# Kernel tuning notes

Measured on AMD Instinct MI355X. Metric: run time of the kernel, lower is better.

The kernel has to match this reference:

```python
import jax, jax.numpy as jnp
import numpy as np

N_HEADS = 8
D_HEAD = 64  # n_embd=512 / n_heads=8


def setup_inputs() -> dict:
    key = jax.random.key(0)
    ks = jax.random.split(key, 5)
    B, T, C = 2, 4096, 512
    x = jax.random.normal(ks[0], (B, T, C), dtype=jnp.float32)
    s = 1.0 / np.sqrt(C)
    Wq = jax.random.normal(ks[1], (C, C), dtype=jnp.float32) * s
    Wk = jax.random.normal(ks[2], (C, C), dtype=jnp.float32) * s
    Wv = jax.random.normal(ks[3], (C, C), dtype=jnp.float32) * s
    Wout = jax.random.normal(ks[4], (C, C), dtype=jnp.float32) * s
    return {"x": x, "Wq": Wq, "Wk": Wk, "Wv": Wv, "Wout": Wout}


def reference(x, Wq, Wk, Wv, Wout):
    # x: [B,T,C]; nn.Linear(y) = y @ W.T, here weights stored as [C,C] used directly
    B, T, C = x.shape
    H, D = N_HEADS, D_HEAD
    q = (x @ Wq.T).reshape(B, T, H, D).transpose(0, 2, 1, 3)  # [B,H,T,D]
    k = (x @ Wk.T).reshape(B, T, H, D).transpose(0, 2, 1, 3)
    v = (x @ Wv.T).reshape(B, T, H, D).transpose(0, 2, 1, 3)
    att = jnp.einsum('bhqd,bhkd->bhqk', q, k) / jnp.sqrt(jnp.float32(D))  # [B,H,T,T]
    causal = jnp.tril(jnp.ones((T, T), dtype=bool))
    att = jnp.where(causal, att, -jnp.inf)
    att = jax.nn.softmax(att, axis=-1)
    # dropout is identity in eval mode (p=0)
    y = jnp.einsum('bhqk,bhkd->bhqd', att, v)  # [B,H,T,D]
    y = y.transpose(0, 2, 1, 3).reshape(B, T, C)
    return y @ Wout.T
```

## Files before the change

kernel.cpp:

```cpp
#include <hip/hip_runtime.h>
#include <hip/hip_bf16.h>
#include <math.h>
#include <stdint.h>

using bf16 = __hip_bfloat16;
typedef __attribute__((ext_vector_type(8))) short short8;
typedef __attribute__((ext_vector_type(4))) short short4v;
typedef __attribute__((ext_vector_type(4))) float float4v;

#define MFMA16(a, b, c) __builtin_amdgcn_mfma_f32_16x16x32_bf16(a, b, c, 0, 0, 0)

__device__ __forceinline__ short bfbits(float f) {
  bf16 h = (bf16)f;
  return *(short*)&h;
}

__device__ __forceinline__ short8 ld_cvt8(const float* p) {
  union { float4v v[2]; float f[8]; } u;
  u.v[0] = *(const float4v*)p;
  u.v[1] = *(const float4v*)(p + 4);
  short8 r;
#pragma unroll
  for (int j = 0; j < 8; j++) r[j] = bfbits(u.f[j]);
  return r;
}

__device__ __forceinline__ void gload16(const bf16* g, bf16* l) {
  __builtin_amdgcn_global_load_lds(
      (const __attribute__((address_space(1))) void*)g,
      (__attribute__((address_space(3))) void*)l, 16, 0, 0);
}

__global__ __launch_bounds__(256) void conv_all(
    const float* __restrict__ x, const float* __restrict__ w0,
    const float* __restrict__ w1, const float* __restrict__ w2,
    const float* __restrict__ w3, bf16* __restrict__ cx,
    bf16* __restrict__ cw) {
  size_t gid = ((size_t)blockIdx.x * 256 + threadIdx.x) * 8;
  const float* src;
  bf16* dst;
  size_t off;
  if (gid < 4194304) {
    src = x; dst = cx; off = gid;
  } else {
    size_t r = gid - 4194304;
    int wi = (int)(r >> 18);
    src = wi == 0 ? w0 : wi == 1 ? w1 : wi == 2 ? w2 : w3;
    dst = cw + ((size_t)wi << 18);
    off = r & 262143;
  }
  *(short8*)(dst + off) = ld_cvt8(src + off);
}

template <int MODE, int MT>
__device__ __forceinline__ void gemm_body(bf16* As, bf16* Bs,
                                          const bf16* __restrict__ A,
                                          const bf16* __restrict__ W,
                                          void* __restrict__ outp,
                                          float oscale) {
  constexpr int MI = MT / 32;
  const int bm = blockIdx.x * MT, bn = blockIdx.y * 128;
  const int tid = threadIdx.x;
  const int lane = tid & 63;
  const int wave = tid >> 6;
  const int lr = lane & 15, quad = lane >> 4;
  const int wm = (wave & 1) * (MT / 2), wn = (wave >> 1) * 64;

  const int srow = lane >> 3;
  const int scl = (lane & 7) ^ (srow & 7);
  const int rsw = lr & 7;

  float4v acc[MI][4] = {};

  for (int k0 = 0; k0 < 512; k0 += 64) {
    __syncthreads();
#pragma unroll
    for (int j = 0; j < MT / 32; j++) {
      const int m = wave + 4 * j;
      gload16(&A[(size_t)(bm + 8 * m + srow) * 512 + k0 + scl * 8],
              &As[(8 * m) * 64]);
    }
#pragma unroll
    for (int j = 0; j < 4; j++) {
      const int m = wave + 4 * j;
      gload16(&W[(size_t)(bn + 8 * m + srow) * 512 + k0 + scl * 8],
              &Bs[(8 * m) * 64]);
    }
    __syncthreads();
#pragma unroll
    for (int kk = 0; kk < 2; kk++) {
      short8 af[MI], bfv[4];
#pragma unroll
      for (int i = 0; i < MI; i++)
        af[i] = *(const short8*)
            &As[(wm + i * 16 + lr) * 64 + ((4 * kk + quad) ^ rsw) * 8];
#pragma unroll
      for (int i = 0; i < 4; i++)
        bfv[i] = *(const short8*)
            &Bs[(wn + i * 16 + lr) * 64 + ((4 * kk + quad) ^ rsw) * 8];
#pragma unroll
      for (int mi = 0; mi < MI; mi++)
#pragma unroll
        for (int ni = 0; ni < 4; ni++)
          acc[mi][ni] = MFMA16(af[mi], bfv[ni], acc[mi][ni]);
    }
  }

  const int row0 = bm + wm + quad * 4;
  const int col0 = bn + wn + lr;
#pragma unroll
  for (int mi = 0; mi < MI; mi++) {
#pragma unroll
    for (int ni = 0; ni < 4; ni++) {
      const int col = col0 + ni * 16;
      if (MODE == 1) {
        float* out = (float*)outp;
#pragma unroll
        for (int i = 0; i < 4; i++) {
          int m = row0 + mi * 16 + i;
          out[(size_t)m * 512 + col] = acc[mi][ni][i];
        }
      } else if (MODE == 0) {
        bf16* out = (bf16*)outp;
        const int hh = col >> 6, d = col & 63;
#pragma unroll
        for (int i = 0; i < 4; i++) {
          int m = row0 + mi * 16 + i;
          int bb = m >> 12, t = m & 4095;
          out[(((size_t)(bb * 8 + hh) * 4096 + t) << 6) + d] =
              (bf16)(acc[mi][ni][i] * oscale);
        }
      } else {
        bf16* out = (bf16*)outp;
        const int hh = col >> 6, d = col & 63;
        int m0 = row0 + mi * 16;
        int bb = m0 >> 12, t0 = m0 & 4095;
        short4v pk;
#pragma unroll
        for (int i = 0; i < 4; i++) pk[i] = bfbits(acc[mi][ni][i]);
        *(short4v*)&out[(((size_t)(bb * 8 + hh) * 64 + d) << 12) + t0] = pk;
      }
    }
  }
}

#define QSCALE 0.18033688f

__global__ __launch_bounds__(256) void qkv_kernel(
    const bf16* __restrict__ cx, const bf16* __restrict__ cW,
    bf16* q, bf16* k, bf16* vt) {
  __shared__ __align__(16) bf16 As[128 * 64];
  __shared__ __align__(16) bf16 Bs[128 * 64];
  if (blockIdx.z == 0)      gemm_body<0, 128>(As, Bs, cx, cW, q, QSCALE);
  else if (blockIdx.z == 1) gemm_body<0, 128>(As, Bs, cx, cW + 262144, k, 1.0f);
  else                      gemm_body<2, 128>(As, Bs, cx, cW + 2 * 262144, vt, 1.0f);
}

__global__ __launch_bounds__(256) void proj_kernel(
    const bf16* __restrict__ y, const bf16* __restrict__ cWout,
    float* __restrict__ out) {
  __shared__ __align__(16) bf16 As[64 * 64];
  __shared__ __align__(16) bf16 Bs[128 * 64];
  gemm_body<1, 64>(As, Bs, y, cWout, out, 1.0f);
}

__device__ __forceinline__ int lsw(int row, int col) {
  return (row << 6) + (col ^ ((row & 7) << 3));
}

template <bool DIAG>
__device__ __forceinline__ void attn_step(const bf16* __restrict__ Kc,
                                          const bf16* __restrict__ Vc,
                                          short8 qf0, short8 qf1, short8 ones,
                                          int wave, int lr, int quad,
                                          float4v& Lacc, float4v* O) {
  float4v S[4] = {};
#pragma unroll
  for (int nc = 0; nc < 4; nc++) {
    short8 kf0 = *(const short8*)&Kc[lsw(nc * 16 + lr, quad * 8)];
    short8 kf1 = *(const short8*)&Kc[lsw(nc * 16 + lr, 32 + quad * 8)];
    S[nc] = MFMA16(kf0, qf0, S[nc]);
    S[nc] = MFMA16(kf1, qf1, S[nc]);
  }

  short8 pf0, pf1;
#pragma unroll
  for (int nc = 0; nc < 4; nc++) {
#pragma unroll
    for (int i = 0; i < 4; i++) {
      float pv = exp2f(S[nc][i]);
      if (DIAG) {
        int kl = nc * 16 + quad * 4 + i;
        pv = (kl > wave * 16 + lr) ? 0.f : pv;
      }
      short bb = bfbits(pv);
      if (nc == 0)      pf0[i] = bb;
      else if (nc == 1) pf0[4 + i] = bb;
      else if (nc == 2) pf1[i] = bb;
      else              pf1[4 + i] = bb;
    }
  }

  Lacc = MFMA16(pf0, ones, Lacc);
  Lacc = MFMA16(pf1, ones, Lacc);

#pragma unroll
  for (int nc = 0; nc < 4; nc++) {
    const int row = nc * 16 + lr;
    short8 vfa = *(const short8*)&Vc[lsw(row, quad * 8)];
    short8 vfb = *(const short8*)&Vc[lsw(row, 32 + quad * 8)];
    O[nc] = MFMA16(pf0, vfa, O[nc]);
    O[nc] = MFMA16(pf1, vfb, O[nc]);
  }
}

__device__ __forceinline__ void vstore_perm(bf16* Vb, int row, int vA,
                                            short8 rv) {
  short4v lo = __builtin_shufflevector(rv, rv, 0, 1, 2, 3);
  short4v hi = __builtin_shufflevector(rv, rv, 4, 5, 6, 7);
  *(short4v*)&Vb[lsw(row, vA)] = lo;
  *(short4v*)&Vb[lsw(row, vA + 8)] = hi;
}

__global__ __launch_bounds__(512, 4) void attn_kernel(const bf16* __restrict__ Qg,
                                                      const bf16* __restrict__ Kg,
                                                      const bf16* __restrict__ Vtg,
                                                      bf16* __restrict__ Y) {
  constexpr int T = 4096;
  __shared__ __align__(16) bf16 KV[2][2][2][64 * 64];

  const int bx = blockIdx.x;
  const int p = bx >> 4;
  const int pB = 63 - p;
  const int hb = bx & 15;
  const int h = hb >> 1, b = hb & 1;
  const size_t ho = ((size_t)(b * 8 + h)) * T * 64;
  const bf16* Qh = Qg + ho;
  const bf16* Kh = Kg + ho;
  const bf16* Vth = Vtg + ho;

  const int tid = threadIdx.x;
  const int G = tid >> 8;
  const int t = tid & 255;
  const int wave = t >> 6, lane = t & 63;
  const int lr = lane & 15, quad = lane >> 4;

  const int hA = (p + 2) >> 1;
  const int hB = (65 - p) >> 1;
  const int myA = G ? (p + 1 - hA) : hA;
  const int myB = G ? (64 - p - hB) : hB;
  const int aB = G ? hA : 0;
  const int bB = G ? hB : 0;
  const int mysteps = myA + myB;

  bf16* const Kb0 = KV[G][0][0];
  bf16* const Kb1 = KV[G][1][0];
  bf16* const Vb0 = KV[G][0][1];
  bf16* const Vb1 = KV[G][1][1];

  const int sr = t >> 3;
  const int s8 = t & 7;
  const int sc = s8 * 8;
  const int vA = 32 * (s8 >> 2) + 16 * (s8 & 1) + 4 * ((s8 >> 1) & 1);
  const bf16* ksrc0 = Kh + (size_t)sr * 64 + sc;
  const bf16* ksrc1 = ksrc0 + 32 * 64;
  const bf16* vsrc0 = Vth + (size_t)sr * T + sc;
  const bf16* vsrc1 = vsrc0 + (size_t)32 * T;
  const int d0 = lsw(sr, sc);
  const int d1 = lsw(sr + 32, sc);

  const int kt0 = (0 < myA) ? aB : bB;

  short8 rk0 = *(const short8*)(ksrc0 + (size_t)kt0 * 4096);
  short8 rk1 = *(const short8*)(ksrc1 + (size_t)kt0 * 4096);
  short8 rv0 = *(const short8*)(vsrc0 + (size_t)kt0 * 64);
  short8 rv1 = *(const short8*)(vsrc1 + (size_t)kt0 * 64);

  {
    int rr = tid >> 3, c = (tid & 7) * 8;
    *(short8*)&KV[0][1][0][lsw(rr, c)] =
        *(const short8*)&Qh[(size_t)(p * 64 + rr) * 64 + c];
    *(short8*)&KV[1][1][0][lsw(rr, c)] =
        *(const short8*)&Qh[(size_t)(pB * 64 + rr) * 64 + c];
  }
  __syncthreads();
  short8 qfA0 = *(const short8*)&KV[0][1][0][lsw(wave * 16 + lr, quad * 8)];
  short8 qfA1 = *(const short8*)&KV[0][1][0][lsw(wave * 16 + lr, 32 + quad * 8)];
  short8 qfB0 = *(const short8*)&KV[1][1][0][lsw(wave * 16 + lr, quad * 8)];
  short8 qfB1 = *(const short8*)&KV[1][1][0][lsw(wave * 16 + lr, 32 + quad * 8)];
  *(short8*)&Kb0[d0] = rk0;
  *(short8*)&Kb0[d1] = rk1;
  vstore_perm(Vb0, sr, vA, rv0);
  vstore_perm(Vb0, sr + 32, vA, rv1);
  __syncthreads();

  short8 ones;
#pragma unroll
  for (int j = 0; j < 8; j++) ones[j] = (short)0x3F80;

  float4v OA[4] = {}, OB[4] = {};
  float4v LA = {}, LB = {};

  for (int s = 0; s < 33; s++) {
    const bool act = s < mysteps;
    const bool pf = s + 1 < mysteps;
    if (pf) {
      const int sn = s + 1;
      const int ktn = (sn < myA) ? (aB + sn) : (bB + (sn - myA));
      rk0 = *(const short8*)(ksrc0 + (size_t)ktn * 4096);
      rk1 = *(const short8*)(ksrc1 + (size_t)ktn * 4096);
      rv0 = *(const short8*)(vsrc0 + (size_t)ktn * 64);
      rv1 = *(const short8*)(vsrc1 + (size_t)ktn * 64);
    }

    if (act) {
      const bf16* Kc = (s & 1) ? Kb1 : Kb0;
      const bf16* Vc = (s & 1) ? Vb1 : Vb0;
      if (s < myA) {
        const int kt = aB + s;
        if (kt == p) attn_step<true>(Kc, Vc, qfA0, qfA1, ones, wave, lr, quad, LA, OA);
        else         attn_step<false>(Kc, Vc, qfA0, qfA1, ones, wave, lr, quad, LA, OA);
      } else {
        const int kt = bB + (s - myA);
        if (kt == pB) attn_step<true>(Kc, Vc, qfB0, qfB1, ones, wave, lr, quad, LB, OB);
        else          attn_step<false>(Kc, Vc, qfB0, qfB1, ones, wave, lr, quad, LB, OB);
      }
    }

    if (pf) {
      bf16* Kn = (s & 1) ? Kb0 : Kb1;
      bf16* Vn = (s & 1) ? Vb0 : Vb1;
      *(short8*)&Kn[d0] = rk0;
      *(short8*)&Kn[d1] = rk1;
      vstore_perm(Vn, sr, vA, rv0);
      vstore_perm(Vn, sr + 32, vA, rv1);
    }
    __syncthreads();
  }

  float* OpA = (float*)&KV[1][0][0][0];
  float* OpB = (float*)&KV[1][1][0][0];
  float* LpA = (float*)&KV[0][0][0][0];
  float* LpB = LpA + 64;
  const int r0 = wave * 16 + quad * 4;
  if (G == 1) {
#pragma unroll
    for (int nc = 0; nc < 4; nc++)
#pragma unroll
      for (int i = 0; i < 4; i++) {
        OpA[(r0 + i) * 64 + nc * 16 + lr] = OA[nc][i];
        OpB[(r0 + i) * 64 + nc * 16 + lr] = OB[nc][i];
      }
    if (lr == 0) {
#pragma unroll
      for (int i = 0; i < 4; i++) { LpA[r0 + i] = LA[i]; LpB[r0 + i] = LB[i]; }
    }
  }
  __syncthreads();
  if (G == 0) {
    float invA[4], invB[4];
#pragma unroll
    for (int i = 0; i < 4; i++) {
      invA[i] = 1.f / (LA[i] + LpA[r0 + i]);
      invB[i] = 1.f / (LB[i] + LpB[r0 + i]);
    }
    const size_t ybA = ((size_t)b * T + p * 64 + r0) * 512 + h * 64;
    const size_t ybB = ((size_t)b * T + pB * 64 + r0) * 512 + h * 64;
#pragma unroll
    for (int nc = 0; nc < 4; nc++)
#pragma unroll
      for (int i = 0; i < 4; i++) {
        float oa = OA[nc][i] + OpA[(r0 + i) * 64 + nc * 16 + lr];
        float ob = OB[nc][i] + OpB[(r0 + i) * 64 + nc * 16 + lr];
        Y[ybA + (size_t)i * 512 + nc * 16 + lr] = (bf16)(oa * invA[i]);
        Y[ybB + (size_t)i * 512 + nc * 16 + lr] = (bf16)(ob * invB[i]);
      }
  }
}

extern "C" void kernel_launch(void* const* d_in, const int* in_sizes, int n_in,
                              void* d_out, int out_size, void* d_ws, size_t ws_size,
                              hipStream_t stream) {
  (void)out_size; (void)ws_size;
  const int NX = 8192 * 512;
  int xi = 0;
  for (int i = 0; i < n_in; i++)
    if (in_sizes[i] == NX) { xi = i; break; }
  const float* x = (const float*)d_in[xi];
  const float* wsrc[4];
  int wn = 0;
  for (int i = 0; i < n_in && wn < 4; i++)
    if (i != xi) wsrc[wn++] = (const float*)d_in[i];

  bf16* ws = (bf16*)d_ws;
  const size_t HE = (size_t)NX;
  bf16* q  = ws;
  bf16* k  = q + HE;
  bf16* yx = k + HE;
  bf16* cw = yx + HE;
  bf16* vt = (bf16*)d_out;
  float* out = (float*)d_out;

  conv_all<<<2560, 256, 0, stream>>>(x, wsrc[0], wsrc[1], wsrc[2], wsrc[3],
                                     yx, cw);
  qkv_kernel<<<dim3(64, 4, 3), 256, 0, stream>>>(yx, cw, q, k, vt);
  attn_kernel<<<512, 512, 0, stream>>>(q, k, vt, yx);
  proj_kernel<<<dim3(128, 4), 256, 0, stream>>>(yx, cw + 3 * 262144, out);
}
```

Measured before the change: 161.5 us.

## Load K tiles directly to LDS, prefetch V two steps ahead, raise MFMA priority

K tiles now go from global memory straight into swizzled LDS through a gload16 direct-to-LDS path instead of being staged in registers. V tiles are prefetched two steps ahead with alternating register buffers, which needs a manually unrolled two-step loop macro. s_setprio raises wave priority around the MFMA sections. The goal is to hide global load latency and cut register staging, at the cost of more registers for the extra V buffers and a dependence on the direct-LDS load ordering being correct with respect to the barriers.

```diff
diff --git a/kernel.cpp b/kernel.cpp
--- a/kernel.cpp
+++ b/kernel.cpp
@@ -175,6 +175,7 @@
                                           int wave, int lr, int quad,
                                           float4v& Lacc, float4v* O) {
   float4v S[4] = {};
+  __builtin_amdgcn_s_setprio(1);
 #pragma unroll
   for (int nc = 0; nc < 4; nc++) {
     short8 kf0 = *(const short8*)&Kc[lsw(nc * 16 + lr, quad * 8)];
@@ -182,6 +183,7 @@
     S[nc] = MFMA16(kf0, qf0, S[nc]);
     S[nc] = MFMA16(kf1, qf1, S[nc]);
   }
+  __builtin_amdgcn_s_setprio(0);
 
   short8 pf0, pf1;
 #pragma unroll
@@ -201,6 +203,7 @@
     }
   }
 
+  __builtin_amdgcn_s_setprio(1);
   Lacc = MFMA16(pf0, ones, Lacc);
   Lacc = MFMA16(pf1, ones, Lacc);
 
@@ -212,6 +215,7 @@
     O[nc] = MFMA16(pf0, vfa, O[nc]);
     O[nc] = MFMA16(pf1, vfb, O[nc]);
   }
+  __builtin_amdgcn_s_setprio(0);
 }
 
 __device__ __forceinline__ void vstore_perm(bf16* Vb, int row, int vA,
@@ -248,33 +252,40 @@
   const int hA = (p + 2) >> 1;
   const int hB = (65 - p) >> 1;
   const int myA = G ? (p + 1 - hA) : hA;
-  const int myB = G ? (64 - p - hB) : hB;
   const int aB = G ? hA : 0;
   const int bB = G ? hB : 0;
-  const int mysteps = myA + myB;
+  const int mysteps = myA + (G ? (64 - p - hB) : hB);
+
+  auto kt_of = [&](int s) { return (s < myA) ? (aB + s) : (bB + (s - myA)); };
 
   bf16* const Kb0 = KV[G][0][0];
   bf16* const Kb1 = KV[G][1][0];
   bf16* const Vb0 = KV[G][0][1];
   bf16* const Vb1 = KV[G][1][1];
 
+  const int srowK = lane >> 3;
+  const int sclK = (lane & 7) ^ (srowK & 7);
+
   const int sr = t >> 3;
   const int s8 = t & 7;
   const int sc = s8 * 8;
   const int vA = 32 * (s8 >> 2) + 16 * (s8 & 1) + 4 * ((s8 >> 1) & 1);
-  const bf16* ksrc0 = Kh + (size_t)sr * 64 + sc;
-  const bf16* ksrc1 = ksrc0 + 32 * 64;
   const bf16* vsrc0 = Vth + (size_t)sr * T + sc;
   const bf16* vsrc1 = vsrc0 + (size_t)32 * T;
-  const int d0 = lsw(sr, sc);
-  const int d1 = lsw(sr + 32, sc);
-
-  const int kt0 = (0 < myA) ? aB : bB;
-
-  short8 rk0 = *(const short8*)(ksrc0 + (size_t)kt0 * 4096);
-  short8 rk1 = *(const short8*)(ksrc1 + (size_t)kt0 * 4096);
-  short8 rv0 = *(const short8*)(vsrc0 + (size_t)kt0 * 64);
-  short8 rv1 = *(const short8*)(vsrc1 + (size_t)kt0 * 64);
+
+  const int kt0 = kt_of(0), kt1 = kt_of(1);
+
+  short8 rvA0 = *(const short8*)(vsrc0 + (size_t)kt0 * 64);
+  short8 rvA1 = *(const short8*)(vsrc1 + (size_t)kt0 * 64);
+  short8 rvB0 = *(const short8*)(vsrc0 + (size_t)kt1 * 64);
+  short8 rvB1 = *(const short8*)(vsrc1 + (size_t)kt1 * 64);
+
+#pragma unroll
+  for (int j = 0; j < 2; j++) {
+    const int rb = wave * 16 + 8 * j;
+    gload16(&Kh[(size_t)(kt0 * 64 + rb + srowK) * 64 + sclK * 8],
+            &Kb0[rb * 64]);
+  }
 
   {
     int rr = tid >> 3, c = (tid & 7) * 8;
@@ -288,10 +299,8 @@
   short8 qfA1 = *(const short8*)&KV[0][1][0][lsw(wave * 16 + lr, 32 + quad * 8)];
   short8 qfB0 = *(const short8*)&KV[1][1][0][lsw(wave * 16 + lr, quad * 8)];
   short8 qfB1 = *(const short8*)&KV[1][1][0][lsw(wave * 16 + lr, 32 + quad * 8)];
-  *(short8*)&Kb0[d0] = rk0;
-  *(short8*)&Kb0[d1] = rk1;
-  vstore_perm(Vb0, sr, vA, rv0);
-  vstore_perm(Vb0, sr + 32, vA, rv1);
+  vstore_perm(Vb0, sr, vA, rvA0);
+  vstore_perm(Vb0, sr + 32, vA, rvA1);
   __syncthreads();
 
   short8 ones;
@@ -301,42 +310,53 @@
   float4v OA[4] = {}, OB[4] = {};
   float4v LA = {}, LB = {};
 
-  for (int s = 0; s < 33; s++) {
-    const bool act = s < mysteps;
-    const bool pf = s + 1 < mysteps;
-    if (pf) {
-      const int sn = s + 1;
-      const int ktn = (sn < myA) ? (aB + sn) : (bB + (sn - myA));
-      rk0 = *(const short8*)(ksrc0 + (size_t)ktn * 4096);
-      rk1 = *(const short8*)(ksrc1 + (size_t)ktn * 4096);
-      rv0 = *(const short8*)(vsrc0 + (size_t)ktn * 64);
-      rv1 = *(const short8*)(vsrc1 + (size_t)ktn * 64);
-    }
-
-    if (act) {
-      const bf16* Kc = (s & 1) ? Kb1 : Kb0;
-      const bf16* Vc = (s & 1) ? Vb1 : Vb0;
-      if (s < myA) {
-        const int kt = aB + s;
-        if (kt == p) attn_step<true>(Kc, Vc, qfA0, qfA1, ones, wave, lr, quad, LA, OA);
-        else         attn_step<false>(Kc, Vc, qfA0, qfA1, ones, wave, lr, quad, LA, OA);
-      } else {
-        const int kt = bB + (s - myA);
-        if (kt == pB) attn_step<true>(Kc, Vc, qfB0, qfB1, ones, wave, lr, quad, LB, OB);
-        else          attn_step<false>(Kc, Vc, qfB0, qfB1, ones, wave, lr, quad, LB, OB);
-      }
-    }
-
-    if (pf) {
-      bf16* Kn = (s & 1) ? Kb0 : Kb1;
-      bf16* Vn = (s & 1) ? Vb0 : Vb1;
-      *(short8*)&Kn[d0] = rk0;
-      *(short8*)&Kn[d1] = rk1;
-      vstore_perm(Vn, sr, vA, rv0);
-      vstore_perm(Vn, sr + 32, vA, rv1);
-    }
-    __syncthreads();
-  }
+#define ASTEP(S, VI0, VI1, VW0, VW1)                                          \
+  {                                                                           \
+    const int _s = (S);                                                       \
+    if (_s + 1 < mysteps) {                                                   \
+      const int ktn = kt_of(_s + 1);                                          \
+      bf16* Kn = (_s & 1) ? Kb0 : Kb1;                                        \
+      _Pragma("unroll")                                                       \
+      for (int j = 0; j < 2; j++) {                                           \
+        const int rb = wave * 16 + 8 * j;                                     \
+        gload16(&Kh[(size_t)(ktn * 64 + rb + srowK) * 64 + sclK * 8],         \
+                &Kn[rb * 64]);                                                \
+      }                                                                       \
+    }                                                                         \
+    if (_s + 2 < mysteps) {                                                   \
+      const int ktn = kt_of(_s + 2);                                          \
+      VI0 = *(const short8*)(vsrc0 + (size_t)ktn * 64);                       \
+      VI1 = *(const short8*)(vsrc1 + (size_t)ktn * 64);                       \
+    }                                                                         \
+    if (_s < mysteps) {                                                       \
+      const bf16* Kc = (_s & 1) ? Kb1 : Kb0;                                  \
+      const bf16* Vc = (_s & 1) ? Vb1 : Vb0;                                  \
+      if (_s < myA) {                                                         \
+        if (aB + _s == p)                                                     \
+          attn_step<true>(Kc, Vc, qfA0, qfA1, ones, wave, lr, quad, LA, OA);  \
+        else                                                                  \
+          attn_step<false>(Kc, Vc, qfA0, qfA1, ones, wave, lr, quad, LA, OA); \
+      } else {                                                                \
+        if (bB + (_s - myA) == pB)                                            \
+          attn_step<true>(Kc, Vc, qfB0, qfB1, ones, wave, lr, quad, LB, OB);  \
+        else                                                                  \
+          attn_step<false>(Kc, Vc, qfB0, qfB1, ones, wave, lr, quad, LB, OB); \
+      }                                                                       \
+    }                                                                         \
+    if (_s + 1 < mysteps) {                                                   \
+      bf16* Vn = (_s & 1) ? Vb0 : Vb1;                                        \
+      vstore_perm(Vn, sr, vA, VW0);                                           \
+      vstore_perm(Vn, sr + 32, vA, VW1);                                      \
+    }                                                                         \
+    __syncthreads();                                                          \
+  }
+
+  for (int s = 0; s < 32; s += 2) {
+    ASTEP(s,     rvA0, rvA1, rvB0, rvB1);
+    ASTEP(s + 1, rvB0, rvB1, rvA0, rvA1);
+  }
+  ASTEP(32, rvA0, rvA1, rvB0, rvB1);
+#undef ASTEP
 
   float* OpA = (float*)&KV[1][0][0][0];
   float* OpB = (float*)&KV[1][1][0][0];
```

Result: slower. 166.7 us (+3.2%).
